# Optimization experiments

Hardware: AMD Instinct MI355X
Metric: run time of the kernel (lower is better)

## Reference

```python
import jax, jax.numpy as jnp
import numpy as np

EPS = 1e-6  # EPSILON in the original (undefined there; small stabilizer)
MS = 1      # max_shift_size
FEAT = 128  # memory_feature_size


def setup_inputs() -> dict:
    key = jax.random.key(0)
    ks = jax.random.split(key, 17)
    B, V, E, H, N, F = 64, 10000, 256, 512, 8192, FEAT
    G = 4 * H
    s = 0.02  # param init scale
    return {
        'x': jax.random.randint(ks[0], (B,), 0, V),
        'h': jax.random.normal(ks[1], (B, H)) * 0.1,
        'c': jax.random.normal(ks[2], (B, H)) * 0.1,
        'w_read': jax.random.uniform(ks[3], (B, N)),
        'w_write': jax.random.uniform(ks[4], (B, N)),
        'bank': jax.random.normal(ks[5], (B, N, F)),
        'emb': jax.random.normal(ks[6], (V, E)) * s,
        'W_ih': jax.random.normal(ks[7], (G, E)) * s,
        'b_ih': jnp.zeros((G,)),
        'W_hh': jax.random.normal(ks[8], (G, H)) * s,
        'b_hh': jnp.zeros((G,)),
        'W_read': jax.random.normal(ks[9], (134, H)) * s,
        'b_read': jnp.zeros((134,)),
        'W_write': jax.random.normal(ks[10], (390, H)) * s,
        'b_write': jnp.zeros((390,)),
        'W_out': jax.random.normal(ks[11], (V, F)) * s,
        'b_out': jnp.zeros((V,)),
    }


def _lstm_cell(xe, h, c, W_ih, b_ih, W_hh, b_hh):
    g = xe @ W_ih.T + b_ih + h @ W_hh.T + b_hh  # [B, 4H]
    i, f, gg, o = jnp.split(g, 4, axis=1)
    c2 = jax.nn.sigmoid(f) * c + jax.nn.sigmoid(i) * jnp.tanh(gg)
    h2 = jax.nn.sigmoid(o) * jnp.tanh(c2)
    return h2, c2


def _head_move(bank, w_prev, k, b, g, s, r):
    # content addressing: cosine similarity of key vs each memory row
    mE = bank + EPS                       # [B, N, F]
    kE = k[:, None, :] + EPS              # [B, 1, F]
    num = jnp.sum(mE * kE, axis=-1)       # [B, N]
    den = jnp.linalg.norm(mE, axis=-1) * jnp.linalg.norm(kE, axis=-1)
    sim = num / jnp.maximum(den, 1e-8)
    w = jax.nn.softmax(b * sim, axis=1)
    # interpolation (as written in the source: w + (1-g)*w_prev)
    w = w + (1.0 - g) * w_prev
    # circular shift by location addressing (vectorized conv over modulo pad)
    N = w.shape[1]
    idx = (jnp.arange(N)[:, None] + jnp.arange(-MS, MS + 1)[None, :]) % N  # [N, K]
    w = jnp.einsum('bnk,bk->bn', w[:, idx], s)
    # sharpen
    wr = w ** r
    return wr / (jnp.sum(wr, axis=1, keepdims=True) + EPS)


def _interpret_read(h, W, b):
    o = h @ W.T + b
    F = FEAT
    k = o[:, :F]
    beta = jax.nn.softplus(o[:, F:F + 1])
    g = jax.nn.sigmoid(o[:, F + 1:F + 2])
    s = jax.nn.softmax(o[:, F + 2:F + 2 + (2 * MS + 1)], axis=1)
    r = 1.0 + jax.nn.softplus(o[:, F + 2 + (2 * MS + 1):F + 3 + (2 * MS + 1)])
    return k, beta, g, s, r


def _interpret_write(h, W, b):
    o = h @ W.T + b
    F = FEAT
    k, beta, g, s, r = _interpret_read(h, W[:F + 3 + (2 * MS + 1)], b[:F + 3 + (2 * MS + 1)])
    base = F + 3 + (2 * MS + 1)
    e = jax.nn.sigmoid(o[:, base:base + F])
    a = o[:, base + F:base + 2 * F]
    return k, beta, g, s, r, e, a


def reference(x, h, c, w_read, w_write, bank, emb, W_ih, b_ih, W_hh, b_hh,
              W_read, b_read, W_write, b_write, W_out, b_out):
    # controller
    xe = emb[x]                                  # [B, E]
    h2, c2 = _lstm_cell(xe, h, c, W_ih, b_ih, W_hh, b_hh)
    # write head + memory write
    k, beta, g, s, r, e, a = _interpret_write(h2, W_write, b_write)
    ww = _head_move(bank, w_write, k, beta, g, s, r)   # [B, N]
    bank2 = bank * (1.0 - ww[:, :, None] * e[:, None, :]) + ww[:, :, None] * a[:, None, :]
    # read head + memory read (uses updated bank)
    k, beta, g, s, r = _interpret_read(h2, W_read, b_read)
    wr = _head_move(bank2, w_read, k, beta, g, s, r)
    rvec = jnp.sum(wr[:, :, None] * bank2, axis=1)     # [B, F]
    return rvec @ W_out.T + b_out                      # [B, V]
```

## Files before the change

### kernel.cpp

```cpp
#include <hip/hip_runtime.h>
#include <math.h>

#define BB   64
#define NN   8192
#define FF   128
#define HH   512
#define GG   2048
#define EE   256
#define VV   10000
#define EPSF 1e-6f

static constexpr size_t OFF_XT    = 0;
static constexpr size_t OFF_GPART = 49152;
static constexpr size_t OFF_H2T   = 311296;
static constexpr size_t OFF_HPART = 344064;
static constexpr size_t OFF_PAR   = 411136;
static constexpr size_t OFF_ZW    = 445952;
static constexpr size_t OFF_Q4    = 970240;
static constexpr size_t OFF_Q1    = 3067392;
static constexpr size_t OFF_WR    = 3591680;
static constexpr size_t OFF_WRWW  = 4115968;
static constexpr size_t OFF_PT    = 4640256;
static constexpr size_t OFF_T3    = 5164544;
static constexpr size_t OFF_RVEC  = 5164608;

__device__ __forceinline__ float sigmoidf_(float x){ return 1.f/(1.f + __expf(-x)); }
__device__ __forceinline__ float softplusf_(float x){ return (x > 20.f) ? x : log1pf(__expf(x)); }

__global__ __launch_bounds__(256) void gather_xt_kernel(
    const int* __restrict__ x, const float* __restrict__ h,
    const float* __restrict__ emb, float* __restrict__ Xt)
{
  const int idx = blockIdx.x*256 + threadIdx.x;
  const int k = idx >> 6, b = idx & 63;
  float v = (k < EE) ? emb[(size_t)x[b]*EE + k] : h[(size_t)b*HH + (k - EE)];
  Xt[(size_t)k*64 + b] = v;
}

__global__ __launch_bounds__(256) void lstm_gates_kernel(
    const float* __restrict__ Xt, const float* __restrict__ Wih,
    const float* __restrict__ Whh, float* __restrict__ gpart)
{
  const int tid = threadIdx.x;
  const int lane = tid & 63;
  const int gw = __builtin_amdgcn_readfirstlane(blockIdx.x*4 + (tid >> 6));
  const int jg = gw >> 1, kc = gw & 1;
  const int j0 = jg << 2;
  float a0=0.f, a1=0.f, a2=0.f, a3=0.f;
  if (kc == 0){
    const float* w0 = Wih + (size_t)(j0+0)*EE;
    const float* w1 = Wih + (size_t)(j0+1)*EE;
    const float* w2 = Wih + (size_t)(j0+2)*EE;
    const float* w3 = Wih + (size_t)(j0+3)*EE;
    #pragma unroll 4
    for (int k = 0; k < EE; ++k){
      const float xv = Xt[(size_t)k*64 + lane];
      a0 = fmaf(w0[k],xv,a0); a1 = fmaf(w1[k],xv,a1);
      a2 = fmaf(w2[k],xv,a2); a3 = fmaf(w3[k],xv,a3);
    }
    const float* v0 = Whh + (size_t)(j0+0)*HH;
    const float* v1 = Whh + (size_t)(j0+1)*HH;
    const float* v2 = Whh + (size_t)(j0+2)*HH;
    const float* v3 = Whh + (size_t)(j0+3)*HH;
    #pragma unroll 4
    for (int k = 0; k < 128; ++k){
      const float xv = Xt[(size_t)(EE+k)*64 + lane];
      a0 = fmaf(v0[k],xv,a0); a1 = fmaf(v1[k],xv,a1);
      a2 = fmaf(v2[k],xv,a2); a3 = fmaf(v3[k],xv,a3);
    }
  } else {
    const float* v0 = Whh + (size_t)(j0+0)*HH;
    const float* v1 = Whh + (size_t)(j0+1)*HH;
    const float* v2 = Whh + (size_t)(j0+2)*HH;
    const float* v3 = Whh + (size_t)(j0+3)*HH;
    #pragma unroll 4
    for (int k = 128; k < 512; ++k){
      const float xv = Xt[(size_t)(EE+k)*64 + lane];
      a0 = fmaf(v0[k],xv,a0); a1 = fmaf(v1[k],xv,a1);
      a2 = fmaf(v2[k],xv,a2); a3 = fmaf(v3[k],xv,a3);
    }
  }
  float* gp = gpart + (size_t)kc*131072 + (size_t)j0*64 + lane;
  gp[0] = a0; gp[64] = a1; gp[128] = a2; gp[192] = a3;
}

__global__ __launch_bounds__(256) void lstm_act_kernel(
    const float* __restrict__ gpart, const float* __restrict__ bih,
    const float* __restrict__ bhh, const float* __restrict__ c,
    float* __restrict__ h2t)
{
  const int idx = blockIdx.x*256 + threadIdx.x;
  const int bb = idx & 63, hh = idx >> 6;
  #define GSUM(j) (gpart[(size_t)(j)*64+bb] + gpart[(size_t)131072+(size_t)(j)*64+bb] + bih[j] + bhh[j])
  const float gi = GSUM(hh);
  const float gf = GSUM(512+hh);
  const float gg = GSUM(1024+hh);
  const float go = GSUM(1536+hh);
  #undef GSUM
  const float c0 = c[(size_t)bb*HH + hh];
  const float c2 = sigmoidf_(gf)*c0 + sigmoidf_(gi)*tanhf(gg);
  h2t[(size_t)hh*64 + bb] = sigmoidf_(go)*tanhf(c2);
}

__global__ __launch_bounds__(256) void head_gemm_kernel(
    const float* __restrict__ h2t, const float* __restrict__ Ww,
    const float* __restrict__ Wr, float* __restrict__ hpart)
{
  const int tid = threadIdx.x;
  const int lane = tid & 63;
  const int gw = __builtin_amdgcn_readfirstlane(blockIdx.x*4 + (tid >> 6));
  const int jg = gw >> 1, kc = gw & 1;
  if (jg >= 131) return;
  const int j0 = jg << 2;
  const float* w0 = (j0+0 < 390) ? (Ww + (size_t)(j0+0)*HH) : (Wr + (size_t)(j0+0-390)*HH);
  const float* w1 = (j0+1 < 390) ? (Ww + (size_t)(j0+1)*HH) : (Wr + (size_t)(j0+1-390)*HH);
  const float* w2 = (j0+2 < 390) ? (Ww + (size_t)(j0+2)*HH) : (Wr + (size_t)(j0+2-390)*HH);
  const float* w3 = (j0+3 < 390) ? (Ww + (size_t)(j0+3)*HH) : (Wr + (size_t)(j0+3-390)*HH);
  const int k0 = kc << 8;
  float a0=0.f, a1=0.f, a2=0.f, a3=0.f;
  #pragma unroll 4
  for (int k = k0; k < k0+256; ++k){
    const float xv = h2t[(size_t)k*64 + lane];
    a0 = fmaf(w0[k],xv,a0); a1 = fmaf(w1[k],xv,a1);
    a2 = fmaf(w2[k],xv,a2); a3 = fmaf(w3[k],xv,a3);
  }
  float* hp = hpart + (size_t)kc*33536 + (size_t)j0*64 + lane;
  hp[0] = a0; hp[64] = a1; hp[128] = a2; hp[192] = a3;
}

__global__ void interpret_kernel(const float* __restrict__ hp,
                                 const float* __restrict__ bw,
                                 const float* __restrict__ br,
                                 float* __restrict__ params)
{
  const int b = blockIdx.x, l = threadIdx.x;
  float* P = params + (size_t)b*544;
  #define OC(j) (hp[(size_t)(j)*64+b] + hp[(size_t)33536+(size_t)(j)*64+b])
  float skw = 0.f, skr = 0.f, sakr = 0.f, sa2 = 0.f;
  #pragma unroll
  for (int f = l; f < 128; f += 64){
    float kwE = OC(f) + bw[f] + EPSF;
    float ee  = sigmoidf_(OC(134+f) + bw[134+f]);
    float aa  = OC(262+f) + bw[262+f];
    float krE = OC(390+f) + br[f] + EPSF;
    P[f] = kwE; P[128+f] = krE; P[256+f] = aa; P[384+f] = ee;
    skw = fmaf(kwE,kwE,skw); skr = fmaf(krE,krE,skr);
    sakr = fmaf(aa,krE,sakr); sa2 = fmaf(aa,aa,sa2);
  }
  #pragma unroll
  for (int m = 32; m >= 1; m >>= 1){
    skw += __shfl_xor(skw,m); skr += __shfl_xor(skr,m);
    sakr += __shfl_xor(sakr,m); sa2 += __shfl_xor(sa2,m);
  }
  if (l == 0){
    P[512+0] = softplusf_(OC(128) + bw[128]);
    P[512+1] = sigmoidf_(OC(129) + bw[129]);
    {
      float x0 = OC(130)+bw[130], x1 = OC(131)+bw[131], x2 = OC(132)+bw[132];
      float mm = fmaxf(x0, fmaxf(x1, x2));
      float e0 = __expf(x0-mm), e1 = __expf(x1-mm), e2 = __expf(x2-mm);
      float s = e0+e1+e2;
      P[512+2] = e0/s; P[512+3] = e1/s; P[512+4] = e2/s;
    }
    P[512+5] = 1.f + softplusf_(OC(133) + bw[133]);
    P[512+6] = softplusf_(OC(518) + br[128]);
    P[512+7] = sigmoidf_(OC(519) + br[129]);
    {
      float x0 = OC(520)+br[130], x1 = OC(521)+br[131], x2 = OC(522)+br[132];
      float mm = fmaxf(x0, fmaxf(x1, x2));
      float e0 = __expf(x0-mm), e1 = __expf(x1-mm), e2 = __expf(x2-mm);
      float s = e0+e1+e2;
      P[512+8] = e0/s; P[512+9] = e1/s; P[512+10] = e2/s;
    }
    P[512+11] = 1.f + softplusf_(OC(523) + br[133]);
    P[512+12] = sqrtf(skw); P[512+13] = sqrtf(skr);
    P[512+14] = sakr;       P[512+15] = sa2;
  }
  #undef OC
}

__global__ __launch_bounds__(256) void pass_a_kernel(
    const float* __restrict__ bank, const float* __restrict__ params,
    float* __restrict__ zw, float4* __restrict__ q4, float* __restrict__ q1)
{
  const int blk = blockIdx.x;
  const int b = blk >> 5, chunk = blk & 31;
  const int tid = threadIdx.x;
  const int wv = tid >> 6, lane = tid & 63;
  const int fslot = lane & 7, rsub = lane >> 3;
  const float* P = params + (size_t)b*544;
  const int fb = fslot << 4;
  float kw[16], kr[16], av[16], ev[16];
  #pragma unroll
  for (int i = 0; i < 16; ++i){
    kw[i] = P[fb+i]; kr[i] = P[128+fb+i]; av[i] = P[256+fb+i]; ev[i] = P[384+fb+i];
  }
  const float beta_w = P[512+0], nkw = P[512+12];
  const float C_akr = P[512+14], Ca2 = P[512+15];

  for (int it = 0; it < 8; it += 2){
    const int n0 = (chunk << 8) + (it << 5) + (wv << 3) + rsub;
    const size_t rowA = (size_t)b*NN + n0;
    const size_t rowB = rowA + 32;
    const float4* mA4 = reinterpret_cast<const float4*>(bank + rowA*FF + fb);
    const float4* mB4 = reinterpret_cast<const float4*>(bank + rowB*FF + fb);
    float va[16], vb[16];
    *reinterpret_cast<float4*>(&va[0])  = mA4[0];
    *reinterpret_cast<float4*>(&va[4])  = mA4[1];
    *reinterpret_cast<float4*>(&va[8])  = mA4[2];
    *reinterpret_cast<float4*>(&va[12]) = mA4[3];
    *reinterpret_cast<float4*>(&vb[0])  = mB4[0];
    *reinterpret_cast<float4*>(&vb[4])  = mB4[1];
    *reinterpret_cast<float4*>(&vb[8])  = mB4[2];
    *reinterpret_cast<float4*>(&vb[12]) = mB4[3];

    #pragma unroll
    for (int half = 0; half < 2; ++half){
      const float* mv = (half == 0) ? va : vb;
      const size_t row = (half == 0) ? rowA : rowB;
      float s1=0.f,s2=0.f,s3=0.f,s4=0.f,s5=0.f,s6=0.f,s7=0.f,s8=0.f;
      #pragma unroll
      for (int i = 0; i < 16; ++i){
        const float m = mv[i], u = m + EPSF, em = ev[i]*m;
        s1 = fmaf(u,kw[i],s1);  s2 = fmaf(u,u,s2);
        s3 = fmaf(u,kr[i],s3);  s4 = fmaf(em,kr[i],s4);
        s5 = fmaf(u,av[i],s5);  s6 = fmaf(u,em,s6);
        s7 = fmaf(av[i],em,s7); s8 = fmaf(em,em,s8);
      }
      #pragma unroll
      for (int mm = 1; mm < 8; mm <<= 1){
        s1 += __shfl_xor(s1,mm); s2 += __shfl_xor(s2,mm);
        s3 += __shfl_xor(s3,mm); s4 += __shfl_xor(s4,mm);
        s5 += __shfl_xor(s5,mm); s6 += __shfl_xor(s6,mm);
        s7 += __shfl_xor(s7,mm); s8 += __shfl_xor(s8,mm);
      }
      if (fslot == 0){
        const float sim = s1 / fmaxf(sqrtf(s2)*nkw, 1e-8f);
        zw[row] = beta_w * sim;
        q4[row] = make_float4(s2, s3, C_akr - s4, s5 - s6);
        q1[row] = Ca2 - 2.f*s7 + s8;
      }
    }
  }
}

__device__ __forceinline__ float blockMaxF(float v, float* red, int tid){
  #pragma unroll
  for (int m = 32; m >= 1; m >>= 1) v = fmaxf(v, __shfl_xor(v,m));
  if ((tid & 63) == 0) red[tid >> 6] = v;
  __syncthreads();
  if (tid < 64){
    float x = (tid < 16) ? red[tid] : -1e30f;
    #pragma unroll
    for (int m = 8; m >= 1; m >>= 1) x = fmaxf(x, __shfl_xor(x,m));
    if (tid == 0) red[16] = x;
  }
  __syncthreads();
  return red[16];
}
__device__ __forceinline__ float blockSumF(float v, float* red, int tid){
  #pragma unroll
  for (int m = 32; m >= 1; m >>= 1) v += __shfl_xor(v,m);
  if ((tid & 63) == 0) red[tid >> 6] = v;
  __syncthreads();
  if (tid < 64){
    float x = (tid < 16) ? red[tid] : 0.f;
    #pragma unroll
    for (int m = 8; m >= 1; m >>= 1) x += __shfl_xor(x,m);
    if (tid == 0) red[16] = x;
  }
  __syncthreads();
  return red[16];
}

__global__ __launch_bounds__(1024) void head_pipeline_kernel(
    const float* __restrict__ zw, const float4* __restrict__ q4,
    const float* __restrict__ q1,
    const float* __restrict__ w_write, const float* __restrict__ w_read,
    const float* __restrict__ params,
    float* __restrict__ wrg, float* __restrict__ wrwwg, float* __restrict__ T3g)
{
  __shared__ float wa[NN];
  __shared__ float red[20];
  const int b = blockIdx.x;
  const int tid = threadIdx.x;
  const float* P = params + (size_t)b*544 + 512;
  const float g_w = P[1], sw0 = P[2], sw1 = P[3], sw2 = P[4], r_w = P[5];
  const float beta_r = P[6], g_r = P[7], sr0 = P[8], sr1 = P[9], sr2 = P[10], r_r = P[11];
  const float nkr = P[13];
  const size_t base = (size_t)b*NN;

  float  zv[8], q1v[8], wwr[8], wrd[8];
  float4 qv[8];
  #pragma unroll
  for (int i = 0; i < 8; ++i){ int n = tid + (i<<10); zv[i]  = zw[base+n]; }
  #pragma unroll
  for (int i = 0; i < 8; ++i){ int n = tid + (i<<10); qv[i]  = q4[base+n]; }
  #pragma unroll
  for (int i = 0; i < 8; ++i){ int n = tid + (i<<10); q1v[i] = q1[base+n]; }
  #pragma unroll
  for (int i = 0; i < 8; ++i){ int n = tid + (i<<10); wwr[i] = w_write[base+n]; }
  #pragma unroll
  for (int i = 0; i < 8; ++i){ int n = tid + (i<<10); wrd[i] = w_read[base+n]; }

  float cv[8], wwv[8];

  float lm = -1e30f;
  #pragma unroll
  for (int i = 0; i < 8; ++i) lm = fmaxf(lm, zv[i]);
  float M = blockMaxF(lm, red, tid);
  float ls = 0.f;
  #pragma unroll
  for (int i = 0; i < 8; ++i){ zv[i] = __expf(zv[i]-M); ls += zv[i]; }
  float S = blockSumF(ls, red, tid);
  const float invS = 1.f/S;
  #pragma unroll
  for (int i = 0; i < 8; ++i){ int n = tid + (i<<10); wa[n] = zv[i]*invS + (1.f-g_w)*wwr[i]; }
  __syncthreads();
  #pragma unroll
  for (int i = 0; i < 8; ++i){ int n = tid + (i<<10);
    cv[i] = sw0*wa[(n+NN-1)&(NN-1)] + sw1*wa[n] + sw2*wa[(n+1)&(NN-1)]; }
  __syncthreads();
  float lp = 0.f;
  #pragma unroll
  for (int i = 0; i < 8; ++i){ cv[i] = __expf(r_w*__logf(cv[i])); lp += cv[i]; }
  float Sp = blockSumF(lp, red, tid);
  float inv = 1.f/(Sp + EPSF);
  #pragma unroll
  for (int i = 0; i < 8; ++i) wwv[i] = cv[i]*inv;

  lm = -1e30f;
  #pragma unroll
  for (int i = 0; i < 8; ++i){
    const float ww = wwv[i];
    const float num = qv[i].y + ww*qv[i].z;
    const float d2  = qv[i].x + 2.f*ww*qv[i].w + ww*ww*q1v[i];
    const float den = sqrtf(d2)*nkr;
    zv[i] = beta_r * (num / fmaxf(den, 1e-8f));
    lm = fmaxf(lm, zv[i]);
  }
  M = blockMaxF(lm, red, tid);
  ls = 0.f;
  #pragma unroll
  for (int i = 0; i < 8; ++i){ zv[i] = __expf(zv[i]-M); ls += zv[i]; }
  S = blockSumF(ls, red, tid);
  const float invS2 = 1.f/S;
  #pragma unroll
  for (int i = 0; i < 8; ++i){ int n = tid + (i<<10); wa[n] = zv[i]*invS2 + (1.f-g_r)*wrd[i]; }
  __syncthreads();
  #pragma unroll
  for (int i = 0; i < 8; ++i){ int n = tid + (i<<10);
    cv[i] = sr0*wa[(n+NN-1)&(NN-1)] + sr1*wa[n] + sr2*wa[(n+1)&(NN-1)]; }
  __syncthreads();
  float lp2 = 0.f;
  #pragma unroll
  for (int i = 0; i < 8; ++i){ cv[i] = __expf(r_r*__logf(cv[i])); lp2 += cv[i]; }
  float Sp2 = blockSumF(lp2, red, tid);
  inv = 1.f/(Sp2 + EPSF);
  float t3 = 0.f;
  #pragma unroll
  for (int i = 0; i < 8; ++i){
    int n = tid + (i<<10);
    const float wr_ = cv[i]*inv;
    wrg[base+n] = wr_;
    const float xx = wr_*wwv[i];
    wrwwg[base+n] = xx;
    t3 += xx;
  }
  float T3 = blockSumF(t3, red, tid);
  if (tid == 0) T3g[b] = T3;
}

__global__ __launch_bounds__(256) void pass_d_kernel(
    const float* __restrict__ bank, const float* __restrict__ wrg,
    const float* __restrict__ wrwwg, float* __restrict__ pT)
{
  const int blk = 2047 - blockIdx.x;
  const int b = blk >> 5, chunk = blk & 31;
  const int tid = threadIdx.x;
  const int st = tid >> 5, li = tid & 31;
  float4 a1 = make_float4(0.f,0.f,0.f,0.f);
  float4 a2 = make_float4(0.f,0.f,0.f,0.f);
  for (int it = 28; it >= 0; it -= 4){
    float w1v[4], w2v[4];
    float4 mv[4];
    #pragma unroll
    for (int u = 0; u < 4; ++u){
      const int n = (chunk << 8) + ((it+u) << 3) + st;
      const size_t row = (size_t)b*NN + n;
      w1v[u] = wrg[row];
      w2v[u] = wrwwg[row];
      mv[u] = reinterpret_cast<const float4*>(bank + row*FF)[li];
    }
    #pragma unroll
    for (int u = 0; u < 4; ++u){
      a1.x = fmaf(w1v[u],mv[u].x,a1.x); a1.y = fmaf(w1v[u],mv[u].y,a1.y);
      a1.z = fmaf(w1v[u],mv[u].z,a1.z); a1.w = fmaf(w1v[u],mv[u].w,a1.w);
      a2.x = fmaf(w2v[u],mv[u].x,a2.x); a2.y = fmaf(w2v[u],mv[u].y,a2.y);
      a2.z = fmaf(w2v[u],mv[u].z,a2.z); a2.w = fmaf(w2v[u],mv[u].w,a2.w);
    }
  }
  __shared__ float lds[8*256];
  *reinterpret_cast<float4*>(&lds[st*256 + li*4]) = a1;
  *reinterpret_cast<float4*>(&lds[st*256 + 128 + li*4]) = a2;
  __syncthreads();
  float s = 0.f;
  #pragma unroll
  for (int k = 0; k < 8; ++k) s += lds[k*256 + tid];
  pT[(size_t)blk*256 + tid] = s;
}

__global__ __launch_bounds__(256) void rvec_kernel(
    const float* __restrict__ pT, const float* __restrict__ params,
    const float* __restrict__ T3g, float* __restrict__ rvec)
{
  const int gid = blockIdx.x*256 + threadIdx.x;
  const int b = gid >> 7, f = gid & 127;
  float t1 = 0.f, t2 = 0.f;
  for (int cc = 0; cc < 32; ++cc){
    const float* p = pT + (size_t)((b<<5) + cc)*256;
    t1 += p[f]; t2 += p[128+f];
  }
  const float* P = params + (size_t)b*544;
  rvec[gid] = t1 - P[384+f]*t2 + P[256+f]*T3g[b];
}

__global__ __launch_bounds__(256) void out_gemm_kernel(
    const float* __restrict__ rvec, const float* __restrict__ Wout,
    const float* __restrict__ bout, float* __restrict__ out)
{
  const int tid = threadIdx.x;
  const int wv = __builtin_amdgcn_readfirstlane(tid >> 6);
  const int lane = tid & 63;
  const int j0 = blockIdx.x*32 + wv*8;
  float acc[8];
  #pragma unroll
  for (int jj = 0; jj < 8; ++jj){ int j = j0 + jj; acc[jj] = (j < VV) ? bout[j] : 0.f; }
  for (int fc = 0; fc < 128; fc += 32){
    float rv[32];
    #pragma unroll
    for (int i = 0; i < 32; ++i) rv[i] = rvec[lane*128 + fc + i];
    #pragma unroll
    for (int jj = 0; jj < 8; ++jj){
      const int j = j0 + jj;
      if (j < VV){
        const float* w = Wout + (size_t)j*128 + fc;
        #pragma unroll
        for (int i = 0; i < 32; ++i) acc[jj] = fmaf(w[i], rv[i], acc[jj]);
      }
    }
  }
  #pragma unroll
  for (int jj = 0; jj < 8; ++jj){
    int j = j0 + jj;
    if (j < VV) out[(size_t)lane*VV + j] = acc[jj];
  }
}

extern "C" void kernel_launch(void* const* d_in, const int* in_sizes, int n_in,
                              void* d_out, int out_size, void* d_ws, size_t ws_size,
                              hipStream_t stream)
{
  const int*   x       = (const int*)  d_in[0];
  const float* h       = (const float*)d_in[1];
  const float* c       = (const float*)d_in[2];
  const float* w_read  = (const float*)d_in[3];
  const float* w_write = (const float*)d_in[4];
  const float* bank    = (const float*)d_in[5];
  const float* emb     = (const float*)d_in[6];
  const float* Wih     = (const float*)d_in[7];
  const float* bih     = (const float*)d_in[8];
  const float* Whh     = (const float*)d_in[9];
  const float* bhh     = (const float*)d_in[10];
  const float* Wr      = (const float*)d_in[11];
  const float* br      = (const float*)d_in[12];
  const float* Ww      = (const float*)d_in[13];
  const float* bw      = (const float*)d_in[14];
  const float* Wout    = (const float*)d_in[15];
  const float* bout    = (const float*)d_in[16];
  float* out = (float*)d_out;
  float* ws  = (float*)d_ws;

  float* Xt    = ws + OFF_XT;
  float* gpart = ws + OFF_GPART;
  float* h2t   = ws + OFF_H2T;
  float* hpart = ws + OFF_HPART;
  float* par   = ws + OFF_PAR;
  float* zwp   = ws + OFF_ZW;
  float4* q4p  = reinterpret_cast<float4*>(ws + OFF_Q4);
  float* q1p   = ws + OFF_Q1;
  float* wrp   = ws + OFF_WR;
  float* wrwwp = ws + OFF_WRWW;
  float* pTp   = ws + OFF_PT;
  float* T3p   = ws + OFF_T3;
  float* rvp   = ws + OFF_RVEC;

  hipLaunchKernelGGL(gather_xt_kernel,     dim3(192),  dim3(256), 0, stream, x, h, emb, Xt);
  hipLaunchKernelGGL(lstm_gates_kernel,    dim3(256),  dim3(256), 0, stream, Xt, Wih, Whh, gpart);
  hipLaunchKernelGGL(lstm_act_kernel,      dim3(128),  dim3(256), 0, stream, gpart, bih, bhh, c, h2t);
  hipLaunchKernelGGL(head_gemm_kernel,     dim3(66),   dim3(256), 0, stream, h2t, Ww, Wr, hpart);
  hipLaunchKernelGGL(interpret_kernel,     dim3(64),   dim3(64),  0, stream, hpart, bw, br, par);
  hipLaunchKernelGGL(pass_a_kernel,        dim3(2048), dim3(256), 0, stream, bank, par, zwp, q4p, q1p);
  hipLaunchKernelGGL(head_pipeline_kernel, dim3(64),   dim3(1024),0, stream, zwp, q4p, q1p, w_write, w_read, par, wrp, wrwwp, T3p);
  hipLaunchKernelGGL(pass_d_kernel,        dim3(2048), dim3(256), 0, stream, bank, wrp, wrwwp, pTp);
  hipLaunchKernelGGL(rvec_kernel,          dim3(32),   dim3(256), 0, stream, pTp, par, T3p, rvp);
  hipLaunchKernelGGL(out_gemm_kernel,      dim3(313),  dim3(256), 0, stream, rvp, Wout, bout, out);
}
```

Measured before the change: 197.0 us.

## Fuse LSTM gate GEMM with activation, drop split-K in head GEMM, interleave bank loads

```diff
diff --git a/kernel.cpp b/kernel.cpp
--- a/kernel.cpp
+++ b/kernel.cpp
@@ -11,18 +11,17 @@
 #define EPSF 1e-6f
 
 static constexpr size_t OFF_XT    = 0;
-static constexpr size_t OFF_GPART = 49152;
-static constexpr size_t OFF_H2T   = 311296;
-static constexpr size_t OFF_HPART = 344064;
-static constexpr size_t OFF_PAR   = 411136;
-static constexpr size_t OFF_ZW    = 445952;
-static constexpr size_t OFF_Q4    = 970240;
-static constexpr size_t OFF_Q1    = 3067392;
-static constexpr size_t OFF_WR    = 3591680;
-static constexpr size_t OFF_WRWW  = 4115968;
-static constexpr size_t OFF_PT    = 4640256;
-static constexpr size_t OFF_T3    = 5164544;
-static constexpr size_t OFF_RVEC  = 5164608;
+static constexpr size_t OFF_OCAT  = 49152;
+static constexpr size_t OFF_PAR   = 82688;
+static constexpr size_t OFF_H2T   = 117504;
+static constexpr size_t OFF_ZW    = 150272;
+static constexpr size_t OFF_Q4    = 674560;
+static constexpr size_t OFF_Q1    = 2771712;
+static constexpr size_t OFF_WR    = 3296000;
+static constexpr size_t OFF_WRWW  = 3820288;
+static constexpr size_t OFF_PT    = 4344576;
+static constexpr size_t OFF_T3    = 4868864;
+static constexpr size_t OFF_RVEC  = 4868928;
 
 __device__ __forceinline__ float sigmoidf_(float x){ return 1.f/(1.f + __expf(-x)); }
 __device__ __forceinline__ float softplusf_(float x){ return (x > 20.f) ? x : log1pf(__expf(x)); }
@@ -37,112 +36,85 @@
   Xt[(size_t)k*64 + b] = v;
 }
 
-__global__ __launch_bounds__(256) void lstm_gates_kernel(
+__global__ __launch_bounds__(256) void lstm_fused_kernel(
     const float* __restrict__ Xt, const float* __restrict__ Wih,
-    const float* __restrict__ Whh, float* __restrict__ gpart)
+    const float* __restrict__ bih, const float* __restrict__ Whh,
+    const float* __restrict__ bhh, const float* __restrict__ c,
+    float* __restrict__ h2t)
+{
+  const int lane = threadIdx.x & 63;
+  const int hh = __builtin_amdgcn_readfirstlane(blockIdx.x*4 + (threadIdx.x >> 6));
+  const float* wi0 = Wih + (size_t)(hh       )*EE;
+  const float* wi1 = Wih + (size_t)(hh +  512)*EE;
+  const float* wi2 = Wih + (size_t)(hh + 1024)*EE;
+  const float* wi3 = Wih + (size_t)(hh + 1536)*EE;
+  float a0=0.f, a1=0.f, a2=0.f, a3=0.f;
+  #pragma unroll 8
+  for (int k = 0; k < EE; ++k){
+    const float xv = Xt[(size_t)k*64 + lane];
+    a0 = fmaf(wi0[k],xv,a0); a1 = fmaf(wi1[k],xv,a1);
+    a2 = fmaf(wi2[k],xv,a2); a3 = fmaf(wi3[k],xv,a3);
+  }
+  const float* wh0 = Whh + (size_t)(hh       )*HH;
+  const float* wh1 = Whh + (size_t)(hh +  512)*HH;
+  const float* wh2 = Whh + (size_t)(hh + 1024)*HH;
+  const float* wh3 = Whh + (size_t)(hh + 1536)*HH;
+  #pragma unroll 8
+  for (int k = 0; k < HH; ++k){
+    const float xv = Xt[(size_t)(EE+k)*64 + lane];
+    a0 = fmaf(wh0[k],xv,a0); a1 = fmaf(wh1[k],xv,a1);
+    a2 = fmaf(wh2[k],xv,a2); a3 = fmaf(wh3[k],xv,a3);
+  }
+  const float gi = a0 + bih[hh]      + bhh[hh];
+  const float gf = a1 + bih[512+hh]  + bhh[512+hh];
+  const float gg = a2 + bih[1024+hh] + bhh[1024+hh];
+  const float go = a3 + bih[1536+hh] + bhh[1536+hh];
+  const float c0 = c[(size_t)lane*HH + hh];
+  const float c2 = sigmoidf_(gf)*c0 + sigmoidf_(gi)*tanhf(gg);
+  h2t[(size_t)hh*64 + lane] = sigmoidf_(go)*tanhf(c2);
+}
+
+__global__ __launch_bounds__(256) void head_gemm_kernel(
+    const float* __restrict__ h2t, const float* __restrict__ Ww,
+    const float* __restrict__ bw, const float* __restrict__ Wr,
+    const float* __restrict__ br, float* __restrict__ ocat)
 {
   const int tid = threadIdx.x;
   const int lane = tid & 63;
-  const int gw = __builtin_amdgcn_readfirstlane(blockIdx.x*4 + (tid >> 6));
-  const int jg = gw >> 1, kc = gw & 1;
-  const int j0 = jg << 2;
-  float a0=0.f, a1=0.f, a2=0.f, a3=0.f;
-  if (kc == 0){
-    const float* w0 = Wih + (size_t)(j0+0)*EE;
-    const float* w1 = Wih + (size_t)(j0+1)*EE;
-    const float* w2 = Wih + (size_t)(j0+2)*EE;
-    const float* w3 = Wih + (size_t)(j0+3)*EE;
-    #pragma unroll 4
-    for (int k = 0; k < EE; ++k){
-      const float xv = Xt[(size_t)k*64 + lane];
-      a0 = fmaf(w0[k],xv,a0); a1 = fmaf(w1[k],xv,a1);
-      a2 = fmaf(w2[k],xv,a2); a3 = fmaf(w3[k],xv,a3);
-    }
-    const float* v0 = Whh + (size_t)(j0+0)*HH;
-    const float* v1 = Whh + (size_t)(j0+1)*HH;
-    const float* v2 = Whh + (size_t)(j0+2)*HH;
-    const float* v3 = Whh + (size_t)(j0+3)*HH;
-    #pragma unroll 4
-    for (int k = 0; k < 128; ++k){
-      const float xv = Xt[(size_t)(EE+k)*64 + lane];
-      a0 = fmaf(v0[k],xv,a0); a1 = fmaf(v1[k],xv,a1);
-      a2 = fmaf(v2[k],xv,a2); a3 = fmaf(v3[k],xv,a3);
-    }
-  } else {
-    const float* v0 = Whh + (size_t)(j0+0)*HH;
-    const float* v1 = Whh + (size_t)(j0+1)*HH;
-    const float* v2 = Whh + (size_t)(j0+2)*HH;
-    const float* v3 = Whh + (size_t)(j0+3)*HH;
-    #pragma unroll 4
-    for (int k = 128; k < 512; ++k){
-      const float xv = Xt[(size_t)(EE+k)*64 + lane];
-      a0 = fmaf(v0[k],xv,a0); a1 = fmaf(v1[k],xv,a1);
-      a2 = fmaf(v2[k],xv,a2); a3 = fmaf(v3[k],xv,a3);
-    }
-  }
-  float* gp = gpart + (size_t)kc*131072 + (size_t)j0*64 + lane;
-  gp[0] = a0; gp[64] = a1; gp[128] = a2; gp[192] = a3;
-}
-
-__global__ __launch_bounds__(256) void lstm_act_kernel(
-    const float* __restrict__ gpart, const float* __restrict__ bih,
-    const float* __restrict__ bhh, const float* __restrict__ c,
-    float* __restrict__ h2t)
-{
-  const int idx = blockIdx.x*256 + threadIdx.x;
-  const int bb = idx & 63, hh = idx >> 6;
-  #define GSUM(j) (gpart[(size_t)(j)*64+bb] + gpart[(size_t)131072+(size_t)(j)*64+bb] + bih[j] + bhh[j])
-  const float gi = GSUM(hh);
-  const float gf = GSUM(512+hh);
-  const float gg = GSUM(1024+hh);
-  const float go = GSUM(1536+hh);
-  #undef GSUM
-  const float c0 = c[(size_t)bb*HH + hh];
-  const float c2 = sigmoidf_(gf)*c0 + sigmoidf_(gi)*tanhf(gg);
-  h2t[(size_t)hh*64 + bb] = sigmoidf_(go)*tanhf(c2);
-}
-
-__global__ __launch_bounds__(256) void head_gemm_kernel(
-    const float* __restrict__ h2t, const float* __restrict__ Ww,
-    const float* __restrict__ Wr, float* __restrict__ hpart)
-{
-  const int tid = threadIdx.x;
-  const int lane = tid & 63;
-  const int gw = __builtin_amdgcn_readfirstlane(blockIdx.x*4 + (tid >> 6));
-  const int jg = gw >> 1, kc = gw & 1;
+  const int jg = __builtin_amdgcn_readfirstlane(blockIdx.x*4 + (tid >> 6));
   if (jg >= 131) return;
   const int j0 = jg << 2;
   const float* w0 = (j0+0 < 390) ? (Ww + (size_t)(j0+0)*HH) : (Wr + (size_t)(j0+0-390)*HH);
   const float* w1 = (j0+1 < 390) ? (Ww + (size_t)(j0+1)*HH) : (Wr + (size_t)(j0+1-390)*HH);
   const float* w2 = (j0+2 < 390) ? (Ww + (size_t)(j0+2)*HH) : (Wr + (size_t)(j0+2-390)*HH);
   const float* w3 = (j0+3 < 390) ? (Ww + (size_t)(j0+3)*HH) : (Wr + (size_t)(j0+3-390)*HH);
-  const int k0 = kc << 8;
-  float a0=0.f, a1=0.f, a2=0.f, a3=0.f;
-  #pragma unroll 4
-  for (int k = k0; k < k0+256; ++k){
+  float a0 = (j0+0 < 390) ? bw[j0+0] : br[j0+0-390];
+  float a1 = (j0+1 < 390) ? bw[j0+1] : br[j0+1-390];
+  float a2 = (j0+2 < 390) ? bw[j0+2] : br[j0+2-390];
+  float a3 = (j0+3 < 390) ? bw[j0+3] : br[j0+3-390];
+  #pragma unroll 8
+  for (int k = 0; k < HH; ++k){
     const float xv = h2t[(size_t)k*64 + lane];
     a0 = fmaf(w0[k],xv,a0); a1 = fmaf(w1[k],xv,a1);
     a2 = fmaf(w2[k],xv,a2); a3 = fmaf(w3[k],xv,a3);
   }
-  float* hp = hpart + (size_t)kc*33536 + (size_t)j0*64 + lane;
-  hp[0] = a0; hp[64] = a1; hp[128] = a2; hp[192] = a3;
-}
-
-__global__ void interpret_kernel(const float* __restrict__ hp,
-                                 const float* __restrict__ bw,
-                                 const float* __restrict__ br,
+  float* oc = ocat + (size_t)j0*64 + lane;
+  oc[0] = a0; oc[64] = a1; oc[128] = a2; oc[192] = a3;
+}
+
+__global__ void interpret_kernel(const float* __restrict__ oc,
                                  float* __restrict__ params)
 {
   const int b = blockIdx.x, l = threadIdx.x;
   float* P = params + (size_t)b*544;
-  #define OC(j) (hp[(size_t)(j)*64+b] + hp[(size_t)33536+(size_t)(j)*64+b])
+  #define OC(j) (oc[(size_t)(j)*64 + b])
   float skw = 0.f, skr = 0.f, sakr = 0.f, sa2 = 0.f;
   #pragma unroll
   for (int f = l; f < 128; f += 64){
-    float kwE = OC(f) + bw[f] + EPSF;
-    float ee  = sigmoidf_(OC(134+f) + bw[134+f]);
-    float aa  = OC(262+f) + bw[262+f];
-    float krE = OC(390+f) + br[f] + EPSF;
+    float kwE = OC(f) + EPSF;
+    float ee  = sigmoidf_(OC(134+f));
+    float aa  = OC(262+f);
+    float krE = OC(390+f) + EPSF;
     P[f] = kwE; P[128+f] = krE; P[256+f] = aa; P[384+f] = ee;
     skw = fmaf(kwE,kwE,skw); skr = fmaf(krE,krE,skr);
     sakr = fmaf(aa,krE,sakr); sa2 = fmaf(aa,aa,sa2);
@@ -153,26 +125,26 @@
     sakr += __shfl_xor(sakr,m); sa2 += __shfl_xor(sa2,m);
   }
   if (l == 0){
-    P[512+0] = softplusf_(OC(128) + bw[128]);
-    P[512+1] = sigmoidf_(OC(129) + bw[129]);
+    P[512+0] = softplusf_(OC(128));
+    P[512+1] = sigmoidf_(OC(129));
     {
-      float x0 = OC(130)+bw[130], x1 = OC(131)+bw[131], x2 = OC(132)+bw[132];
+      float x0 = OC(130), x1 = OC(131), x2 = OC(132);
       float mm = fmaxf(x0, fmaxf(x1, x2));
       float e0 = __expf(x0-mm), e1 = __expf(x1-mm), e2 = __expf(x2-mm);
       float s = e0+e1+e2;
       P[512+2] = e0/s; P[512+3] = e1/s; P[512+4] = e2/s;
     }
-    P[512+5] = 1.f + softplusf_(OC(133) + bw[133]);
-    P[512+6] = softplusf_(OC(518) + br[128]);
-    P[512+7] = sigmoidf_(OC(519) + br[129]);
+    P[512+5] = 1.f + softplusf_(OC(133));
+    P[512+6] = softplusf_(OC(518));
+    P[512+7] = sigmoidf_(OC(519));
     {
-      float x0 = OC(520)+br[130], x1 = OC(521)+br[131], x2 = OC(522)+br[132];
+      float x0 = OC(520), x1 = OC(521), x2 = OC(522);
       float mm = fmaxf(x0, fmaxf(x1, x2));
       float e0 = __expf(x0-mm), e1 = __expf(x1-mm), e2 = __expf(x2-mm);
       float s = e0+e1+e2;
       P[512+8] = e0/s; P[512+9] = e1/s; P[512+10] = e2/s;
     }
-    P[512+11] = 1.f + softplusf_(OC(523) + br[133]);
+    P[512+11] = 1.f + softplusf_(OC(523));
     P[512+12] = sqrtf(skw); P[512+13] = sqrtf(skr);
     P[512+14] = sakr;       P[512+15] = sa2;
   }
@@ -189,30 +161,33 @@
   const int wv = tid >> 6, lane = tid & 63;
   const int fslot = lane & 7, rsub = lane >> 3;
   const float* P = params + (size_t)b*544;
-  const int fb = fslot << 4;
   float kw[16], kr[16], av[16], ev[16];
   #pragma unroll
-  for (int i = 0; i < 16; ++i){
-    kw[i] = P[fb+i]; kr[i] = P[128+fb+i]; av[i] = P[256+fb+i]; ev[i] = P[384+fb+i];
+  for (int i = 0; i < 4; ++i){
+    #pragma unroll
+    for (int j = 0; j < 4; ++j){
+      const int idx = 32*i + 4*fslot + j;
+      kw[4*i+j] = P[idx];     kr[4*i+j] = P[128+idx];
+      av[4*i+j] = P[256+idx]; ev[4*i+j] = P[384+idx];
+    }
   }
   const float beta_w = P[512+0], nkw = P[512+12];
   const float C_akr = P[512+14], Ca2 = P[512+15];
+  const int eoff = 4*fslot;
 
   for (int it = 0; it < 8; it += 2){
     const int n0 = (chunk << 8) + (it << 5) + (wv << 3) + rsub;
     const size_t rowA = (size_t)b*NN + n0;
     const size_t rowB = rowA + 32;
-    const float4* mA4 = reinterpret_cast<const float4*>(bank + rowA*FF + fb);
-    const float4* mB4 = reinterpret_cast<const float4*>(bank + rowB*FF + fb);
+    const float* pA = bank + rowA*FF + eoff;
+    const float* pB = bank + rowB*FF + eoff;
     float va[16], vb[16];
-    *reinterpret_cast<float4*>(&va[0])  = mA4[0];
-    *reinterpret_cast<float4*>(&va[4])  = mA4[1];
-    *reinterpret_cast<float4*>(&va[8])  = mA4[2];
-    *reinterpret_cast<float4*>(&va[12]) = mA4[3];
-    *reinterpret_cast<float4*>(&vb[0])  = mB4[0];
-    *reinterpret_cast<float4*>(&vb[4])  = mB4[1];
-    *reinterpret_cast<float4*>(&vb[8])  = mB4[2];
-    *reinterpret_cast<float4*>(&vb[12]) = mB4[3];
+    #pragma unroll
+    for (int i = 0; i < 4; ++i)
+      *reinterpret_cast<float4*>(&va[4*i]) = *reinterpret_cast<const float4*>(pA + 32*i);
+    #pragma unroll
+    for (int i = 0; i < 4; ++i)
+      *reinterpret_cast<float4*>(&vb[4*i]) = *reinterpret_cast<const float4*>(pB + 32*i);
 
     #pragma unroll
     for (int half = 0; half < 2; ++half){
@@ -482,10 +457,9 @@
   float* ws  = (float*)d_ws;
 
   float* Xt    = ws + OFF_XT;
-  float* gpart = ws + OFF_GPART;
+  float* ocat  = ws + OFF_OCAT;
+  float* par   = ws + OFF_PAR;
   float* h2t   = ws + OFF_H2T;
-  float* hpart = ws + OFF_HPART;
-  float* par   = ws + OFF_PAR;
   float* zwp   = ws + OFF_ZW;
   float4* q4p  = reinterpret_cast<float4*>(ws + OFF_Q4);
   float* q1p   = ws + OFF_Q1;
@@ -496,10 +470,9 @@
   float* rvp   = ws + OFF_RVEC;
 
   hipLaunchKernelGGL(gather_xt_kernel,     dim3(192),  dim3(256), 0, stream, x, h, emb, Xt);
-  hipLaunchKernelGGL(lstm_gates_kernel,    dim3(256),  dim3(256), 0, stream, Xt, Wih, Whh, gpart);
-  hipLaunchKernelGGL(lstm_act_kernel,      dim3(128),  dim3(256), 0, stream, gpart, bih, bhh, c, h2t);
-  hipLaunchKernelGGL(head_gemm_kernel,     dim3(66),   dim3(256), 0, stream, h2t, Ww, Wr, hpart);
-  hipLaunchKernelGGL(interpret_kernel,     dim3(64),   dim3(64),  0, stream, hpart, bw, br, par);
+  hipLaunchKernelGGL(lstm_fused_kernel,    dim3(128),  dim3(256), 0, stream, Xt, Wih, bih, Whh, bhh, c, h2t);
+  hipLaunchKernelGGL(head_gemm_kernel,     dim3(33),   dim3(256), 0, stream, h2t, Ww, bw, Wr, br, ocat);
+  hipLaunchKernelGGL(interpret_kernel,     dim3(64),   dim3(64),  0, stream, ocat, par);
   hipLaunchKernelGGL(pass_a_kernel,        dim3(2048), dim3(256), 0, stream, bank, par, zwp, q4p, q1p);
   hipLaunchKernelGGL(head_pipeline_kernel, dim3(64),   dim3(1024),0, stream, zwp, q4p, q1p, w_write, w_read, par, wrp, wrwwp, T3p);
   hipLaunchKernelGGL(pass_d_kernel,        dim3(2048), dim3(256), 0, stream, bank, wrp, wrwwp, pTp);
```

Result: slower. 235.3 us (+19.4%).
